# Kernel tuning notes

Measured on AMD Instinct MI355X. Metric: run time of the kernel, lower is better.

## Reference

```python
import jax, jax.numpy as jnp
import numpy as np

EMBED_DIM = 1024
NUM_HEADS = 16
HEAD_DIM = EMBED_DIM // NUM_HEADS
B, T = 2, 2048


def setup_inputs() -> dict:
    key = jax.random.key(0)
    ks = jax.random.split(key, 9)
    s = 1.0 / np.sqrt(EMBED_DIM)
    return {
        "x": jax.random.normal(ks[0], (B, T, EMBED_DIM), dtype=jnp.float32),
        "W_q": jax.random.uniform(ks[1], (EMBED_DIM, EMBED_DIM), jnp.float32, -s, s),
        "b_q": jax.random.uniform(ks[2], (EMBED_DIM,), jnp.float32, -s, s),
        "W_k": jax.random.uniform(ks[3], (EMBED_DIM, EMBED_DIM), jnp.float32, -s, s),
        "b_k": jax.random.uniform(ks[4], (EMBED_DIM,), jnp.float32, -s, s),
        "W_v": jax.random.uniform(ks[5], (EMBED_DIM, EMBED_DIM), jnp.float32, -s, s),
        "b_v": jax.random.uniform(ks[6], (EMBED_DIM,), jnp.float32, -s, s),
        "W_o": jax.random.uniform(ks[7], (EMBED_DIM, EMBED_DIM), jnp.float32, -s, s),
        "b_o": jax.random.uniform(ks[8], (EMBED_DIM,), jnp.float32, -s, s),
    }


def reference(x, W_q, b_q, W_k, b_k, W_v, b_v, W_o, b_o):
    Bv, Tv, C = x.shape
    # QKV projections (torch Linear: x @ W.T + b); split into heads -> (B,H,T,Dh)
    def proj(W, b):
        return (x @ W.T + b).reshape(Bv, Tv, NUM_HEADS, HEAD_DIM).transpose(0, 2, 1, 3)
    q, k, v = proj(W_q, b_q), proj(W_k, b_k), proj(W_v, b_v)
    scale = 1.0 / np.sqrt(HEAD_DIM).astype(np.float32)
    scores = jnp.einsum("bhqd,bhkd->bhqk", q, k) * scale  # (B,H,T,T)
    causal = jnp.tril(jnp.ones((Tv, Tv), dtype=bool))
    scores = jnp.where(causal, scores, -jnp.inf)
    attn = jax.nn.softmax(scores, axis=-1)
    # dropout is identity in eval / p=0
    out = jnp.einsum("bhqk,bhkd->bhqd", attn, v)  # (B,H,T,Dh)
    out = out.transpose(0, 2, 1, 3).reshape(Bv, Tv, C)
    return out @ W_o.T + b_o
```

## Files before the change

### kernel.cpp

```cpp
#include <hip/hip_runtime.h>
#include <hip/hip_bf16.h>


typedef __bf16 bf16;
typedef __attribute__((ext_vector_type(8))) __bf16 bf16x8;
typedef __attribute__((ext_vector_type(4))) __bf16 bf16x4;
typedef __attribute__((ext_vector_type(4))) float floatx4;
typedef __attribute__((ext_vector_type(4))) short short4v;

#define LOG2E 1.44269504088896340736f

__device__ __forceinline__ void gl2lds16(const void* g, void* l) {
  __builtin_amdgcn_global_load_lds((const __attribute__((address_space(1))) void*)g,
                                   (__attribute__((address_space(3))) void*)l, 16, 0, 0);
}

__device__ __forceinline__ floatx4 mfma16(bf16x4 a, bf16x4 b, floatx4 c) {
#if __has_builtin(__builtin_amdgcn_mfma_f32_16x16x16_bf16)
  return __builtin_amdgcn_mfma_f32_16x16x16_bf16(a, b, c, 0, 0, 0);
#elif __has_builtin(__builtin_amdgcn_mfma_f32_16x16x16bf16_1k)
  return __builtin_amdgcn_mfma_f32_16x16x16bf16_1k(
      __builtin_bit_cast(short4v, a), __builtin_bit_cast(short4v, b), c, 0, 0, 0);
#else
  floatx4 d = c;
  asm volatile("v_mfma_f32_16x16x16_bf16 %0, %1, %2, %0"
               : "+v"(d) : "v"(a), "v"(b));
  return d;
#endif
}

__global__ __launch_bounds__(256) void cast_all(
    const float* __restrict__ x, const float* __restrict__ wq,
    const float* __restrict__ wk, const float* __restrict__ wv,
    const float* __restrict__ wo, bf16* __restrict__ dst)
{
  const size_t M1 = (size_t)1 << 20;
  size_t i4 = ((size_t)blockIdx.x * 256 + threadIdx.x) * 4;
  const float* src = x;
  size_t off = i4;
  if (i4 >= 4 * M1) {
    size_t r = i4 - 4 * M1;
    int seg = (int)(r >> 20);
    off = r & (M1 - 1);
    src = (seg == 0) ? wq : (seg == 1) ? wk : (seg == 2) ? wv : wo;
  }
  float4 f = *(const float4*)(src + off);
  bf16x4 o = { (bf16)f.x, (bf16)f.y, (bf16)f.z, (bf16)f.w };
  *(bf16x4*)(dst + i4) = o;
}

template<bool F32OUT, bool QKV, int BN>
__global__ __launch_bounds__(256, 3) void gemm_bt(
    const bf16* __restrict__ A, const bf16* __restrict__ Wb,
    const float* __restrict__ bq, const float* __restrict__ bk,
    const float* __restrict__ bv, void* __restrict__ outb,
    bf16* __restrict__ vt, int M, int N, int K, float qscale)
{
  __shared__ bf16 As[128 * 64];
  __shared__ bf16 Bs[BN * 64];
  const int tid = threadIdx.x;
  const int lane = tid & 63;
  const int wid = tid >> 6;
  const int l15 = lane & 15, l4 = lane >> 4;
  constexpr int I = (BN == 128) ? 4 : 2;
  const int wr = (BN == 128) ? (wid >> 1) : wid;
  const int wc = (BN == 128) ? (wid & 1) : 0;

  const bf16* W;
  const float* bias;
  float osc = 1.0f;
  int n0, mat = 0;
  bf16* outh;
  float* outf;
  if (QKV) {
    mat = blockIdx.x >> 3;
    n0 = (blockIdx.x & 7) << 7;
    W = Wb + ((size_t)mat << 20);
    bias = (mat == 0) ? bq : (mat == 1 ? bk : bv);
    if (mat == 0) osc = qscale;
    outh = (bf16*)outb + ((size_t)mat << 22);
    outf = nullptr;
  } else {
    n0 = blockIdx.x * BN;
    W = Wb;
    bias = bq;
    outf = (float*)outb;
    outh = nullptr;
  }
  const int m0 = blockIdx.y << 7;

  floatx4 acc[I][4] = {};

  for (int k0 = 0; k0 < K; k0 += 64) {
#pragma unroll
    for (int it = 0; it < 4; ++it) {
      int c = it * 256 + tid;
      int row = c >> 3, gs = ((c & 7) ^ (row & 7)) << 3;
      gl2lds16(A + (size_t)(m0 + row) * K + k0 + gs, As + c * 8);
    }
#pragma unroll
    for (int it = 0; it < BN / 32; ++it) {
      int c = it * 256 + tid;
      int row = c >> 3, gs = ((c & 7) ^ (row & 7)) << 3;
      gl2lds16(W + (size_t)(n0 + row) * K + k0 + gs, Bs + c * 8);
    }
    __syncthreads();
#pragma unroll
    for (int kk = 0; kk < 2; ++kk) {
      bf16x8 af[I], bfr[4];
#pragma unroll
      for (int i = 0; i < I; ++i) {
        int r = wr * (I * 16) + i * 16 + l15;
        int g = (kk * 4 + l4) ^ (r & 7);
        af[i] = *(const bf16x8*)(As + r * 64 + g * 8);
      }
#pragma unroll
      for (int j = 0; j < 4; ++j) {
        int r = wc * 64 + j * 16 + l15;
        int g = (kk * 4 + l4) ^ (r & 7);
        bfr[j] = *(const bf16x8*)(Bs + r * 64 + g * 8);
      }
#pragma unroll
      for (int i = 0; i < I; ++i)
#pragma unroll
        for (int j = 0; j < 4; ++j)
          acc[i][j] = __builtin_amdgcn_mfma_f32_16x16x32_bf16(af[i], bfr[j], acc[i][j], 0, 0, 0);
    }
    __syncthreads();
  }

  if (QKV && mat == 2) {
#pragma unroll
    for (int j = 0; j < 4; ++j) {
      int col = n0 + wc * 64 + j * 16 + l15;
      float bv_ = bias[col];
      int h = col >> 6, d = col & 63;
#pragma unroll
      for (int i = 0; i < I; ++i) {
        int row = m0 + wr * (I * 16) + i * 16 + l4 * 4;
        int bb = row >> 11, t = row & 2047;
        int tp = (t & ~31) | (((t >> 2) & 3) << 3) | (((t >> 4) & 1) << 2);
        bf16x4 pk;
#pragma unroll
        for (int rg = 0; rg < 4; ++rg) pk[rg] = (bf16)(acc[i][j][rg] + bv_);
        *(bf16x4*)(vt + (((size_t)(bb * 16 + h)) << 17) + ((size_t)d << 11) + tp) = pk;
      }
    }
    return;
  }

#pragma unroll
  for (int j = 0; j < 4; ++j) {
    int col = n0 + wc * 64 + j * 16 + l15;
    float bv_ = bias[col];
#pragma unroll
    for (int i = 0; i < I; ++i) {
#pragma unroll
      for (int rg = 0; rg < 4; ++rg) {
        int row = m0 + wr * (I * 16) + i * 16 + l4 * 4 + rg;
        float v = (acc[i][j][rg] + bv_) * osc;
        if (F32OUT) outf[(size_t)row * N + col] = v;
        else        outh[(size_t)row * N + col] = (bf16)v;
      }
    }
  }
}

__global__ __launch_bounds__(256, 3) void attn_kernel(
    const bf16* __restrict__ Q, const bf16* __restrict__ Kg,
    const bf16* __restrict__ Vt, bf16* __restrict__ AO)
{
  constexpr int T = 2048, C = 1024;
  __shared__ bf16 Ks[2][64 * 64];
  __shared__ bf16 Vts[2][64 * 64];

  const int tid = threadIdx.x;
  const int lane = tid & 63;
  const int w = tid >> 6;
  const int l15 = lane & 15, l4 = lane >> 4;

  const int u = blockIdx.x;
  const int bh = u & 31;
  const int qt = 31 - (u >> 5);
  const int q0 = qt << 6;
  const int nkt = qt + 1;
  const size_t base = ((size_t)(bh >> 4) * T) * C + (bh & 15) * 64;
  const bf16* vtb = Vt + ((size_t)bh << 17);

  auto stageK = [&](int j0, int bufi) {
#pragma unroll
    for (int it = 0; it < 2; ++it) {
      int c = it * 256 + tid;
      int row = c >> 3, g = (c & 7) ^ (row & 7);
      gl2lds16(Kg + base + (size_t)(j0 + row) * C + g * 8, &Ks[bufi][c * 8]);
    }
  };
  auto stageV = [&](int j0, int bufi) {
#pragma unroll
    for (int it = 0; it < 2; ++it) {
      int c = it * 256 + tid;
      int d = c >> 3, g = (c & 7) ^ (d & 7);
      gl2lds16(vtb + ((size_t)d << 11) + j0 + g * 8, &Vts[bufi][c * 8]);
    }
  };

  const int q = q0 + w * 16 + l15;

  bf16x8 qf[2];
  {
    const bf16* qp = Q + base + (size_t)q * C + l4 * 8;
    qf[0] = *(const bf16x8*)(qp);
    qf[1] = *(const bf16x8*)(qp + 32);
  }

  floatx4 o[4] = {};
  float lpart = 0.f;

  stageK(0, 0);
  stageV(0, 0);

  for (int jt = 0; jt < nkt; ++jt) {
    __syncthreads();
    const int cur = jt & 1;
    if (jt + 1 < nkt) {
      stageK((jt + 1) << 6, cur ^ 1);
      stageV((jt + 1) << 6, cur ^ 1);
    }
    const int j0 = jt << 6;

    floatx4 s4[4] = {};
#pragma unroll
    for (int kk = 0; kk < 2; ++kk) {
#pragma unroll
      for (int tj = 0; tj < 4; ++tj) {
        int r = tj * 16 + l15;
        int g = (kk * 4 + l4) ^ (r & 7);
        bf16x8 kf = *(const bf16x8*)(&Ks[cur][r * 64 + g * 8]);
        s4[tj] = __builtin_amdgcn_mfma_f32_16x16x32_bf16(kf, qf[kk], s4[tj], 0, 0, 0);
      }
    }

    if (jt == nkt - 1) {
#pragma unroll
      for (int tj = 0; tj < 4; ++tj) {
        int j = j0 + tj * 16 + l4 * 4;
#pragma unroll
        for (int rg = 0; rg < 4; ++rg)
          if (j + rg > q) s4[tj][rg] = -3e38f;
      }
    }

#pragma unroll
    for (int tj = 0; tj < 4; ++tj)
#pragma unroll
      for (int rg = 0; rg < 4; ++rg) {
        float e = __builtin_amdgcn_exp2f(s4[tj][rg]);
        s4[tj][rg] = e;
        lpart += e;
      }

    bf16x4 pf[4];
#pragma unroll
    for (int tj = 0; tj < 4; ++tj) {
      bf16x4 pk = { (bf16)s4[tj][0], (bf16)s4[tj][1],
                    (bf16)s4[tj][2], (bf16)s4[tj][3] };
      pf[tj] = pk;
    }

#pragma unroll
    for (int tk = 0; tk < 2; ++tk) {
#pragma unroll
      for (int td = 0; td < 4; ++td) {
        int r = td * 16 + l15;
        int g = (tk * 4 + l4) ^ (r & 7);
        bf16x8 vf = *(const bf16x8*)(&Vts[cur][r * 64 + g * 8]);
        bf16x4 lo = { vf[0], vf[1], vf[2], vf[3] };
        bf16x4 hi = { vf[4], vf[5], vf[6], vf[7] };
        o[td] = mfma16(lo, pf[tk * 2], o[td]);
        o[td] = mfma16(hi, pf[tk * 2 + 1], o[td]);
      }
    }
  }

  lpart += __shfl_xor(lpart, 16, 64);
  lpart += __shfl_xor(lpart, 32, 64);
  float inv = 1.0f / lpart;
#pragma unroll
  for (int td = 0; td < 4; ++td) {
    bf16x4 ok = { (bf16)(o[td][0] * inv), (bf16)(o[td][1] * inv),
                  (bf16)(o[td][2] * inv), (bf16)(o[td][3] * inv) };
    *(bf16x4*)(AO + base + (size_t)q * C + td * 16 + l4 * 4) = ok;
  }
}

extern "C" void kernel_launch(void* const* d_in, const int* in_sizes, int n_in,
                              void* d_out, int out_size, void* d_ws, size_t ws_size,
                              hipStream_t stream) {
  const float* x  = (const float*)d_in[0];
  const float* Wq = (const float*)d_in[1];
  const float* bq = (const float*)d_in[2];
  const float* Wk = (const float*)d_in[3];
  const float* bk = (const float*)d_in[4];
  const float* Wv = (const float*)d_in[5];
  const float* bv = (const float*)d_in[6];
  const float* Wo = (const float*)d_in[7];
  const float* bo = (const float*)d_in[8];

  bf16* ws = (bf16*)d_ws;
  const size_t M1 = (size_t)1 << 20;
  bf16* xb  = ws;
  bf16* wqb = ws + 4 * M1;
  bf16* wob = ws + 7 * M1;
  bf16* Qp  = ws + 8 * M1;
  bf16* Vtp = ws + 16 * M1;
  bf16* AOp = ws + 20 * M1;

  cast_all<<<8192, 256, 0, stream>>>(x, Wq, Wk, Wv, Wo, ws);
  gemm_bt<false, true, 128><<<dim3(24, 32), 256, 0, stream>>>(
      xb, wqb, bq, bk, bv, (void*)Qp, Vtp, 4096, 1024, 1024, 0.125f * LOG2E);
  attn_kernel<<<1024, 256, 0, stream>>>(Qp, Qp + 4 * M1, Vtp, AOp);
  gemm_bt<true, false, 64><<<dim3(16, 32), 256, 0, stream>>>(
      AOp, wob, bo, nullptr, nullptr, d_out, nullptr, 4096, 1024, 1024, 1.0f);
}
```

Baseline: 170.7 us.

## Fuse Q, K, V projections into one GEMM block sharing the activation tile

Replaces the templated GEMM with a dedicated QKV kernel. Each block loads one 128x64 activation tile and multiplies it against three 64-wide weight tiles (Q, K and V) in the same k-loop, so x is read from global memory once per column tile instead of three times. The out-projection gets its own simplified kernel with the same 128x64 tiling as before. The trade-off is three times the accumulators (96 floats per thread), a lower occupancy bound of 2 and a grid of 512 blocks instead of 768, which may reduce latency hiding.

```diff
diff --git a/kernel.cpp b/kernel.cpp
--- a/kernel.cpp
+++ b/kernel.cpp
@@ -49,47 +49,23 @@
   *(bf16x4*)(dst + i4) = o;
 }
 
-template<bool F32OUT, bool QKV, int BN>
-__global__ __launch_bounds__(256, 3) void gemm_bt(
+__global__ __launch_bounds__(256, 2) void gemm_qkv(
     const bf16* __restrict__ A, const bf16* __restrict__ Wb,
     const float* __restrict__ bq, const float* __restrict__ bk,
-    const float* __restrict__ bv, void* __restrict__ outb,
-    bf16* __restrict__ vt, int M, int N, int K, float qscale)
+    const float* __restrict__ bv, bf16* __restrict__ Qout,
+    bf16* __restrict__ Kout, bf16* __restrict__ vt, float qscale)
 {
+  constexpr int K = 1024;
   __shared__ bf16 As[128 * 64];
-  __shared__ bf16 Bs[BN * 64];
+  __shared__ bf16 Bs[3][64 * 64];
   const int tid = threadIdx.x;
   const int lane = tid & 63;
   const int wid = tid >> 6;
   const int l15 = lane & 15, l4 = lane >> 4;
-  constexpr int I = (BN == 128) ? 4 : 2;
-  const int wr = (BN == 128) ? (wid >> 1) : wid;
-  const int wc = (BN == 128) ? (wid & 1) : 0;
-
-  const bf16* W;
-  const float* bias;
-  float osc = 1.0f;
-  int n0, mat = 0;
-  bf16* outh;
-  float* outf;
-  if (QKV) {
-    mat = blockIdx.x >> 3;
-    n0 = (blockIdx.x & 7) << 7;
-    W = Wb + ((size_t)mat << 20);
-    bias = (mat == 0) ? bq : (mat == 1 ? bk : bv);
-    if (mat == 0) osc = qscale;
-    outh = (bf16*)outb + ((size_t)mat << 22);
-    outf = nullptr;
-  } else {
-    n0 = blockIdx.x * BN;
-    W = Wb;
-    bias = bq;
-    outf = (float*)outb;
-    outh = nullptr;
-  }
+  const int n0 = blockIdx.x << 6;
   const int m0 = blockIdx.y << 7;
 
-  floatx4 acc[I][4] = {};
+  floatx4 acc[3][2][4] = {};
 
   for (int k0 = 0; k0 < K; k0 += 64) {
 #pragma unroll
@@ -99,7 +75,92 @@
       gl2lds16(A + (size_t)(m0 + row) * K + k0 + gs, As + c * 8);
     }
 #pragma unroll
-    for (int it = 0; it < BN / 32; ++it) {
+    for (int mat = 0; mat < 3; ++mat)
+#pragma unroll
+      for (int it = 0; it < 2; ++it) {
+        int c = it * 256 + tid;
+        int row = c >> 3, gs = ((c & 7) ^ (row & 7)) << 3;
+        gl2lds16(Wb + ((size_t)mat << 20) + (size_t)(n0 + row) * K + k0 + gs,
+                 &Bs[mat][c * 8]);
+      }
+    __syncthreads();
+#pragma unroll
+    for (int kk = 0; kk < 2; ++kk) {
+      bf16x8 af[2];
+#pragma unroll
+      for (int i = 0; i < 2; ++i) {
+        int r = wid * 32 + i * 16 + l15;
+        int g = (kk * 4 + l4) ^ (r & 7);
+        af[i] = *(const bf16x8*)(As + r * 64 + g * 8);
+      }
+#pragma unroll
+      for (int mat = 0; mat < 3; ++mat) {
+        bf16x8 bfr[4];
+#pragma unroll
+        for (int j = 0; j < 4; ++j) {
+          int r = j * 16 + l15;
+          int g = (kk * 4 + l4) ^ (r & 7);
+          bfr[j] = *(const bf16x8*)(&Bs[mat][r * 64 + g * 8]);
+        }
+#pragma unroll
+        for (int i = 0; i < 2; ++i)
+#pragma unroll
+          for (int j = 0; j < 4; ++j)
+            acc[mat][i][j] = __builtin_amdgcn_mfma_f32_16x16x32_bf16(
+                af[i], bfr[j], acc[mat][i][j], 0, 0, 0);
+      }
+    }
+    __syncthreads();
+  }
+
+#pragma unroll
+  for (int j = 0; j < 4; ++j) {
+    int col = n0 + j * 16 + l15;
+    float bq_ = bq[col], bk_ = bk[col], bv_ = bv[col];
+    int h = col >> 6, d = col & 63;
+#pragma unroll
+    for (int i = 0; i < 2; ++i) {
+      int rbase = m0 + wid * 32 + i * 16 + l4 * 4;
+#pragma unroll
+      for (int rg = 0; rg < 4; ++rg) {
+        int row = rbase + rg;
+        Qout[(size_t)row * 1024 + col] = (bf16)((acc[0][i][j][rg] + bq_) * qscale);
+        Kout[(size_t)row * 1024 + col] = (bf16)(acc[1][i][j][rg] + bk_);
+      }
+      int bb = rbase >> 11, t = rbase & 2047;
+      int tp = (t & ~31) | (((t >> 2) & 3) << 3) | (((t >> 4) & 1) << 2);
+      bf16x4 pk;
+#pragma unroll
+      for (int rg = 0; rg < 4; ++rg) pk[rg] = (bf16)(acc[2][i][j][rg] + bv_);
+      *(bf16x4*)(vt + (((size_t)(bb * 16 + h)) << 17) + ((size_t)d << 11) + tp) = pk;
+    }
+  }
+}
+
+__global__ __launch_bounds__(256, 3) void gemm_out(
+    const bf16* __restrict__ A, const bf16* __restrict__ W,
+    const float* __restrict__ bias, float* __restrict__ outf, int K, int N)
+{
+  __shared__ bf16 As[128 * 64];
+  __shared__ bf16 Bs[64 * 64];
+  const int tid = threadIdx.x;
+  const int lane = tid & 63;
+  const int wid = tid >> 6;
+  const int l15 = lane & 15, l4 = lane >> 4;
+  const int n0 = blockIdx.x << 6;
+  const int m0 = blockIdx.y << 7;
+
+  floatx4 acc[2][4] = {};
+
+  for (int k0 = 0; k0 < K; k0 += 64) {
+#pragma unroll
+    for (int it = 0; it < 4; ++it) {
+      int c = it * 256 + tid;
+      int row = c >> 3, gs = ((c & 7) ^ (row & 7)) << 3;
+      gl2lds16(A + (size_t)(m0 + row) * K + k0 + gs, As + c * 8);
+    }
+#pragma unroll
+    for (int it = 0; it < 2; ++it) {
       int c = it * 256 + tid;
       int row = c >> 3, gs = ((c & 7) ^ (row & 7)) << 3;
       gl2lds16(W + (size_t)(n0 + row) * K + k0 + gs, Bs + c * 8);
@@ -107,21 +168,21 @@
     __syncthreads();
 #pragma unroll
     for (int kk = 0; kk < 2; ++kk) {
-      bf16x8 af[I], bfr[4];
-#pragma unroll
-      for (int i = 0; i < I; ++i) {
-        int r = wr * (I * 16) + i * 16 + l15;
+      bf16x8 af[2], bfr[4];
+#pragma unroll
+      for (int i = 0; i < 2; ++i) {
+        int r = wid * 32 + i * 16 + l15;
         int g = (kk * 4 + l4) ^ (r & 7);
         af[i] = *(const bf16x8*)(As + r * 64 + g * 8);
       }
 #pragma unroll
       for (int j = 0; j < 4; ++j) {
-        int r = wc * 64 + j * 16 + l15;
+        int r = j * 16 + l15;
         int g = (kk * 4 + l4) ^ (r & 7);
         bfr[j] = *(const bf16x8*)(Bs + r * 64 + g * 8);
       }
 #pragma unroll
-      for (int i = 0; i < I; ++i)
+      for (int i = 0; i < 2; ++i)
 #pragma unroll
         for (int j = 0; j < 4; ++j)
           acc[i][j] = __builtin_amdgcn_mfma_f32_16x16x32_bf16(af[i], bfr[j], acc[i][j], 0, 0, 0);
@@ -129,40 +190,17 @@
     __syncthreads();
   }
 
-  if (QKV && mat == 2) {
-#pragma unroll
-    for (int j = 0; j < 4; ++j) {
-      int col = n0 + wc * 64 + j * 16 + l15;
-      float bv_ = bias[col];
-      int h = col >> 6, d = col & 63;
-#pragma unroll
-      for (int i = 0; i < I; ++i) {
-        int row = m0 + wr * (I * 16) + i * 16 + l4 * 4;
-        int bb = row >> 11, t = row & 2047;
-        int tp = (t & ~31) | (((t >> 2) & 3) << 3) | (((t >> 4) & 1) << 2);
-        bf16x4 pk;
-#pragma unroll
-        for (int rg = 0; rg < 4; ++rg) pk[rg] = (bf16)(acc[i][j][rg] + bv_);
-        *(bf16x4*)(vt + (((size_t)(bb * 16 + h)) << 17) + ((size_t)d << 11) + tp) = pk;
-      }
-    }
-    return;
-  }
-
 #pragma unroll
   for (int j = 0; j < 4; ++j) {
-    int col = n0 + wc * 64 + j * 16 + l15;
-    float bv_ = bias[col];
-#pragma unroll
-    for (int i = 0; i < I; ++i) {
+    int col = n0 + j * 16 + l15;
+    float b_ = bias[col];
+#pragma unroll
+    for (int i = 0; i < 2; ++i)
 #pragma unroll
       for (int rg = 0; rg < 4; ++rg) {
-        int row = m0 + wr * (I * 16) + i * 16 + l4 * 4 + rg;
-        float v = (acc[i][j][rg] + bv_) * osc;
-        if (F32OUT) outf[(size_t)row * N + col] = v;
-        else        outh[(size_t)row * N + col] = (bf16)v;
-      }
-    }
+        int row = m0 + wid * 32 + i * 16 + l4 * 4 + rg;
+        outf[(size_t)row * N + col] = acc[i][j][rg] + b_;
+      }
   }
 }
 
@@ -312,13 +350,14 @@
   bf16* wqb = ws + 4 * M1;
   bf16* wob = ws + 7 * M1;
   bf16* Qp  = ws + 8 * M1;
+  bf16* Kp  = ws + 12 * M1;
   bf16* Vtp = ws + 16 * M1;
   bf16* AOp = ws + 20 * M1;
 
   cast_all<<<8192, 256, 0, stream>>>(x, Wq, Wk, Wv, Wo, ws);
-  gemm_bt<false, true, 128><<<dim3(24, 32), 256, 0, stream>>>(
-      xb, wqb, bq, bk, bv, (void*)Qp, Vtp, 4096, 1024, 1024, 0.125f * LOG2E);
-  attn_kernel<<<1024, 256, 0, stream>>>(Qp, Qp + 4 * M1, Vtp, AOp);
-  gemm_bt<true, false, 64><<<dim3(16, 32), 256, 0, stream>>>(
-      AOp, wob, bo, nullptr, nullptr, d_out, nullptr, 4096, 1024, 1024, 1.0f);
-}
+  gemm_qkv<<<dim3(16, 32), 256, 0, stream>>>(
+      xb, wqb, bq, bk, bv, Qp, Kp, Vtp, 0.125f * LOG2E);
+  attn_kernel<<<1024, 256, 0, stream>>>(Qp, Kp, Vtp, AOp);
+  gemm_out<<<dim3(16, 32), 256, 0, stream>>>(
+      AOp, wob, bo, (float*)d_out, 1024, 1024);
+}
```

Result: no change. 167.4 us (-1.9%).
